# Performance work log

Hardware: AMD Instinct MI355X
Metric: run time of the kernel (lower is better)

Reference implementation:

```python
import jax, jax.numpy as jnp
import numpy as np

B, N, D, H, L = 2, 2048, 512, 8, 2
HD = D // H


def setup_inputs() -> dict:
    key = jax.random.key(0)
    ks = jax.random.split(key, 8)
    s = 0.02
    return {
        "inputs_embeds": jax.random.normal(ks[0], (B, N, D), jnp.float32),
        "pos_emb": jax.random.normal(ks[1], (N, D), jnp.float32) * s,
        "c_attn_w": jax.random.normal(ks[2], (L, D, 3 * D), jnp.float32) * s,
        "c_attn_b": jnp.zeros((L, 3 * D), jnp.float32),
        "out_w": jax.random.normal(ks[3], (L, D, D), jnp.float32) * s,
        "out_b": jnp.zeros((L, D), jnp.float32),
        "ln1_g": jnp.ones((L, D), jnp.float32),
        "ln1_b": jnp.zeros((L, D), jnp.float32),
        "c_fc_w": jax.random.normal(ks[4], (L, D, 4 * D), jnp.float32) * s,
        "c_fc_b": jnp.zeros((L, 4 * D), jnp.float32),
        "c_proj_w": jax.random.normal(ks[5], (L, 4 * D, D), jnp.float32) * s,
        "c_proj_b": jnp.zeros((L, D), jnp.float32),
        "ln2_g": jnp.ones((L, D), jnp.float32),
        "ln2_b": jnp.zeros((L, D), jnp.float32),
    }


def _layernorm(x, g, b, eps=1e-5):
    mu = jnp.mean(x, axis=-1, keepdims=True)
    var = jnp.mean(jnp.square(x - mu), axis=-1, keepdims=True)
    return (x - mu) * jax.lax.rsqrt(var + eps) * g + b


def _gelu_new(x):
    # NewGELUActivation: tanh approximation
    return 0.5 * x * (1.0 + jnp.tanh(jnp.sqrt(2.0 / jnp.pi) * (x + 0.044715 * x ** 3)))


def _attention(x, w_qkv, b_qkv, w_out, b_out, self_mask):
    qkv = x @ w_qkv + b_qkv                      # [B,N,3D]
    q, k, v = jnp.split(qkv, 3, axis=-1)
    def heads(t):
        return t.reshape(B, N, H, HD).transpose(0, 2, 1, 3)  # [B,H,N,HD]
    q, k, v = heads(q), heads(k), heads(v)
    scores = jnp.einsum('bhqd,bhkd->bhqk', q, k) / jnp.sqrt(jnp.float32(HD))
    neg = jnp.finfo(scores.dtype).min
    scores = jnp.where(self_mask, scores, neg)   # exclude-self mask
    attn = jax.nn.softmax(scores, axis=-1)
    o = jnp.einsum('bhqk,bhkd->bhqd', attn, v)
    o = o.transpose(0, 2, 1, 3).reshape(B, N, D)
    return o @ w_out + b_out


def reference(inputs_embeds, pos_emb, c_attn_w, c_attn_b, out_w, out_b,
              ln1_g, ln1_b, c_fc_w, c_fc_b, c_proj_w, c_proj_b, ln2_g, ln2_b):
    self_mask = ~jnp.eye(N, dtype=bool)[None, None]  # [1,1,N,N]
    h = inputs_embeds + pos_emb[None]
    for l in range(L):
        res = h
        x = _layernorm(h, ln1_g[l], ln1_b[l])
        h = _attention(x, c_attn_w[l], c_attn_b[l], out_w[l], out_b[l], self_mask) + res
        res = h
        x = _layernorm(h, ln2_g[l], ln2_b[l])
        x = _gelu_new(x @ c_fc_w[l] + c_fc_b[l])
        h = (x @ c_proj_w[l] + c_proj_b[l]) + res
    return h
```

## Files before the change

kernel.cpp:

```cpp
#include <hip/hip_runtime.h>
#include <hip/hip_bf16.h>
#include <math.h>

#define BB 2
#define NN 2048
#define DD 512
#define HH 8
#define LL 2
#define TT (BB*NN)

typedef short short8 __attribute__((ext_vector_type(8)));
typedef float floatx4 __attribute__((ext_vector_type(4)));

__device__ __forceinline__ unsigned short f2b(float v) {
    union { float f; unsigned u; } x; x.f = v;
    unsigned r = x.u + 0x7fff + ((x.u >> 16) & 1);
    return (unsigned short)(r >> 16);
}

__device__ __forceinline__ unsigned fbits(float v) {
    union { float f; unsigned u; } x; x.f = v; return x.u;
}

__device__ __forceinline__ unsigned pk_bf16_rtz(float a, float b) {
#if __has_builtin(__builtin_amdgcn_perm)
    return __builtin_amdgcn_perm(fbits(b), fbits(a), 0x07060302);
#else
    return (fbits(b) & 0xFFFF0000u) | (fbits(a) >> 16);
#endif
}

__global__ __launch_bounds__(256) void k_embed(const float* __restrict__ emb,
                                               const float* __restrict__ pos,
                                               float* __restrict__ h) {
    int i = blockIdx.x * 256 + threadIdx.x;
    h[i] = emb[i] + pos[i & (NN * DD - 1)];
}

__global__ __launch_bounds__(256) void k_bias_add(const float* __restrict__ src,
                                                  const float* __restrict__ bias,
                                                  float* __restrict__ dst) {
    int i = blockIdx.x * 256 + threadIdx.x;
    dst[i] = src[i] + bias[i & (DD - 1)];
}

__global__ __launch_bounds__(256) void k_ln(const float* __restrict__ hin,
                                            unsigned short* __restrict__ xout,
                                            const float* __restrict__ g,
                                            const float* __restrict__ b) {
    __shared__ float red[4];
    __shared__ float bc1, bc2;
    int t = blockIdx.x;
    int tid = threadIdx.x;
    int lane = tid & 63, wv = tid >> 6;
    const float* row = hin + (size_t)t * DD;
    float v0 = row[tid];
    float v1 = row[tid + 256];

    float s = v0 + v1;
#pragma unroll
    for (int o = 32; o; o >>= 1) s += __shfl_down(s, o, 64);
    if (lane == 0) red[wv] = s;
    __syncthreads();
    if (tid == 0) bc1 = (red[0] + red[1] + red[2] + red[3]) * (1.0f / DD);
    __syncthreads();
    float mu = bc1;
    float d0 = v0 - mu, d1 = v1 - mu;
    s = d0 * d0 + d1 * d1;
#pragma unroll
    for (int o = 32; o; o >>= 1) s += __shfl_down(s, o, 64);
    if (lane == 0) red[wv] = s;
    __syncthreads();
    if (tid == 0) bc2 = (red[0] + red[1] + red[2] + red[3]) * (1.0f / DD);
    __syncthreads();
    float rstd = rsqrtf(bc2 + 1e-5f);
    xout[(size_t)t * DD + tid]       = f2b(d0 * rstd * g[tid] + b[tid]);
    xout[(size_t)t * DD + tid + 256] = f2b(d1 * rstd * g[tid + 256] + b[tid + 256]);
}

__device__ __forceinline__ float gelu_new(float v) {
    const float c = 0.7978845608028654f;
    float u = c * (v + 0.044715f * v * v * v);
    return 0.5f * v * (1.0f + tanhf(u));
}

#define PL 3145728
__global__ __launch_bounds__(256) void k_wt_all(const float* __restrict__ c_attn_w,
                                                const float* __restrict__ out_w,
                                                const float* __restrict__ c_fc_w,
                                                const float* __restrict__ c_proj_w,
                                                unsigned short* __restrict__ wbuf) {
    __shared__ unsigned short t[64][72];
    int bx = blockIdx.x;
    int l = bx / 768;
    int r = bx - l * 768;
    const float* W; unsigned short* WT; int K, N;
    if (r < 192)      { W = c_attn_w + (size_t)l * 512 * 1536; WT = wbuf + (size_t)l * PL;           K = 512;  N = 1536; }
    else if (r < 256) { r -= 192; W = out_w  + (size_t)l * 512 * 512;  WT = wbuf + (size_t)l * PL + 786432;  K = 512;  N = 512; }
    else if (r < 512) { r -= 256; W = c_fc_w + (size_t)l * 512 * 2048; WT = wbuf + (size_t)l * PL + 1048576; K = 512;  N = 2048; }
    else              { r -= 512; W = c_proj_w + (size_t)l * 2048 * 512; WT = wbuf + (size_t)l * PL + 2097152; K = 2048; N = 512; }
    int tiles_n = N >> 6;
    int n0 = (r % tiles_n) * 64, k0 = (r / tiles_n) * 64;

    int tid = threadIdx.x;
    int rr = tid >> 2;
    int c0 = (tid & 3) * 16;
    const float* src = W + (size_t)(k0 + rr) * N + n0 + c0;
#pragma unroll
    for (int u = 0; u < 4; u++) {
        float4 v = *(const float4*)&src[u * 4];
        t[c0 + u * 4 + 0][rr] = f2b(v.x);
        t[c0 + u * 4 + 1][rr] = f2b(v.y);
        t[c0 + u * 4 + 2][rr] = f2b(v.z);
        t[c0 + u * 4 + 3][rr] = f2b(v.w);
    }
    __syncthreads();
    unsigned short* dst = WT + (size_t)(n0 + rr) * K + k0 + c0;
#pragma unroll
    for (int u = 0; u < 4; u++)
        *(uint2*)&dst[u * 4] = *(const uint2*)&t[rr][c0 + u * 4];
}

template <int ACT, int BF16OUT, int ATOMIC>
__global__ __launch_bounds__(256) void k_mgemm(const unsigned short* __restrict__ Ab,
                                               const unsigned short* __restrict__ Bt,
                                               const float* __restrict__ bias,
                                               float* __restrict__ Cp,
                                               unsigned short* __restrict__ Cb,
                                               int Kfull, int Kchunk, int N) {
    __shared__ unsigned short Als[2][8 * 512];
    __shared__ unsigned short Bls[2][8 * 512];

    int tid = threadIdx.x;
    int l = tid & 63, w = tid >> 6;
    int wm = w >> 1, wn = w & 1;
    int m0 = blockIdx.y * 128, n0 = blockIdx.x * 128;
    int kb = blockIdx.z * Kchunk;
    int lr = l & 15;
    int lk = (l >> 4) * 8;

    const unsigned short* Ap0 = Ab + (size_t)(m0 + (w * 2 + 0) * 16 + lr) * Kfull + kb + lk;
    const unsigned short* Ap1 = Ab + (size_t)(m0 + (w * 2 + 1) * 16 + lr) * Kfull + kb + lk;
    const unsigned short* Bp0 = Bt + (size_t)(n0 + (w * 2 + 0) * 16 + lr) * Kfull + kb + lk;
    const unsigned short* Bp1 = Bt + (size_t)(n0 + (w * 2 + 1) * 16 + lr) * Kfull + kb + lk;
    int la0 = (w * 2 + 0) * 512 + l * 8;
    int la1 = (w * 2 + 1) * 512 + l * 8;

    floatx4 acc[4][4];
#pragma unroll
    for (int i = 0; i < 4; i++)
#pragma unroll
        for (int j = 0; j < 4; j++) acc[i][j] = (floatx4){0.f, 0.f, 0.f, 0.f};

    int nit = Kchunk >> 5;

    uint4 ra0 = *(const uint4*)Ap0;
    uint4 ra1 = *(const uint4*)Ap1;
    uint4 rb0 = *(const uint4*)Bp0;
    uint4 rb1 = *(const uint4*)Bp1;
    *(uint4*)&Als[0][la0] = ra0;
    *(uint4*)&Als[0][la1] = ra1;
    *(uint4*)&Bls[0][la0] = rb0;
    *(uint4*)&Bls[0][la1] = rb1;
    if (nit > 1) {
        ra0 = *(const uint4*)(Ap0 + 32);
        ra1 = *(const uint4*)(Ap1 + 32);
        rb0 = *(const uint4*)(Bp0 + 32);
        rb1 = *(const uint4*)(Bp1 + 32);
    }
    __syncthreads();

    for (int it = 0; it < nit; it++) {
        int c = it & 1;
        if (it + 1 < nit) {
            *(uint4*)&Als[c ^ 1][la0] = ra0;
            *(uint4*)&Als[c ^ 1][la1] = ra1;
            *(uint4*)&Bls[c ^ 1][la0] = rb0;
            *(uint4*)&Bls[c ^ 1][la1] = rb1;
        }
        if (it + 2 < nit) {
            int ko = (it + 2) << 5;
            ra0 = *(const uint4*)(Ap0 + ko);
            ra1 = *(const uint4*)(Ap1 + ko);
            rb0 = *(const uint4*)(Bp0 + ko);
            rb1 = *(const uint4*)(Bp1 + ko);
        }
        short8 a[4], b[4];
#pragma unroll
        for (int i = 0; i < 4; i++) {
            a[i] = *(const short8*)&Als[c][(wm * 4 + i) * 512 + l * 8];
            b[i] = *(const short8*)&Bls[c][(wn * 4 + i) * 512 + l * 8];
        }
#pragma unroll
        for (int i = 0; i < 4; i++)
#pragma unroll
            for (int j = 0; j < 4; j++)
                acc[i][j] = __builtin_amdgcn_mfma_f32_16x16x32_bf16(a[i], b[j], acc[i][j], 0, 0, 0);
        __syncthreads();
    }

    int col_in = l & 15, rquad = (l >> 4) * 4;
    bool addb = (!ATOMIC) || (bias != nullptr && blockIdx.z == 0);
#pragma unroll
    for (int i = 0; i < 4; i++) {
        int gm_base = m0 + wm * 64 + i * 16 + rquad;
#pragma unroll
        for (int j = 0; j < 4; j++) {
            int gn = n0 + wn * 64 + j * 16 + col_in;
            float bv = addb ? bias[gn] : 0.0f;
#pragma unroll
            for (int r = 0; r < 4; r++) {
                size_t off = (size_t)(gm_base + r) * N + gn;
                if (ATOMIC) {
                    atomicAdd(&Cp[off], acc[i][j][r] + bv);
                } else {
                    float v = acc[i][j][r] + bv;
                    if (ACT) v = gelu_new(v);
                    if (BF16OUT) Cb[off] = f2b(v);
                    else Cp[off] = v;
                }
            }
        }
    }
}

__global__ __launch_bounds__(256) void k_attn_mfma(const unsigned short* __restrict__ qkv,
                                                   unsigned short* __restrict__ xatt) {
    __shared__ unsigned short Ks[2][64 * 72];
    __shared__ unsigned short Vt[2][64 * 72];
    __shared__ unsigned short Pls[64 * 72];

    int qt = blockIdx.x, hd = blockIdx.y, b = blockIdx.z;
    int tid = threadIdx.x;
    int l = tid & 63, w = tid >> 6;
    int lr = l & 15, quad = l >> 4;

    const size_t base = (size_t)b * NN * 1536;

    short8 qf[2];
    {
        const unsigned short* qrow = qkv + base + (size_t)(qt * 64 + w * 16 + lr) * 1536 + hd * 64;
        qf[0] = *(const short8*)&qrow[quad * 8];
        qf[1] = *(const short8*)&qrow[quad * 8 + 32];
    }
    short8 onef;
#pragma unroll
    for (int i = 0; i < 8; i++) onef[i] = (short)0x3F80;

    floatx4 O[4];
#pragma unroll
    for (int jd = 0; jd < 4; jd++) O[jd] = (floatx4){0.f, 0.f, 0.f, 0.f};
    floatx4 sacc = (floatx4){0.f, 0.f, 0.f, 0.f};

    int sr = tid >> 2, sc = (tid & 3) * 16;
    int vk = (tid & 15) * 4, vd = (tid >> 4) * 4;
    const unsigned short* Kbase = qkv + base + 512 + hd * 64;
    const unsigned short* Vbase = qkv + base + 1024 + hd * 64;

    uint4 rk0 = *(const uint4*)&Kbase[(size_t)sr * 1536 + sc];
    uint4 rk1 = *(const uint4*)&Kbase[(size_t)sr * 1536 + sc + 8];
    union { uint2 u; unsigned short s[4]; } rv[4];
#pragma unroll
    for (int i = 0; i < 4; i++)
        rv[i].u = *(const uint2*)&Vbase[(size_t)(vk + i) * 1536 + vd];
    *(uint4*)&Ks[0][sr * 72 + sc]     = rk0;
    *(uint4*)&Ks[0][sr * 72 + sc + 8] = rk1;
#pragma unroll
    for (int j = 0; j < 4; j++) {
        union { uint2 u; unsigned short s[4]; } pk;
        pk.s[0] = rv[0].s[j]; pk.s[1] = rv[1].s[j];
        pk.s[2] = rv[2].s[j]; pk.s[3] = rv[3].s[j];
        *(uint2*)&Vt[0][(vd + j) * 72 + vk] = pk.u;
    }
    {
        rk0 = *(const uint4*)&Kbase[(size_t)(64 + sr) * 1536 + sc];
        rk1 = *(const uint4*)&Kbase[(size_t)(64 + sr) * 1536 + sc + 8];
#pragma unroll
        for (int i = 0; i < 4; i++)
            rv[i].u = *(const uint2*)&Vbase[(size_t)(64 + vk + i) * 1536 + vd];
    }
    __syncthreads();

    const float C1 = 0.18033688f;
    const float C2 = -11.5415603f;
    int mq = w * 16 + lr;

    for (int kt = 0; kt < 32; kt++) {
        int c = kt & 1;
        if (kt < 31) {
            *(uint4*)&Ks[c ^ 1][sr * 72 + sc]     = rk0;
            *(uint4*)&Ks[c ^ 1][sr * 72 + sc + 8] = rk1;
#pragma unroll
            for (int j = 0; j < 4; j++) {
                union { uint2 u; unsigned short s[4]; } pk;
                pk.s[0] = rv[0].s[j]; pk.s[1] = rv[1].s[j];
                pk.s[2] = rv[2].s[j]; pk.s[3] = rv[3].s[j];
                *(uint2*)&Vt[c ^ 1][(vd + j) * 72 + vk] = pk.u;
            }
        }
        if (kt < 30) {
            int kn = (kt + 2) * 64;
            rk0 = *(const uint4*)&Kbase[(size_t)(kn + sr) * 1536 + sc];
            rk1 = *(const uint4*)&Kbase[(size_t)(kn + sr) * 1536 + sc + 8];
#pragma unroll
            for (int i = 0; i < 4; i++)
                rv[i].u = *(const uint2*)&Vbase[(size_t)(kn + vk + i) * 1536 + vd];
        }

        floatx4 s[4];
#pragma unroll
        for (int jn = 0; jn < 4; jn++) s[jn] = (floatx4){0.f, 0.f, 0.f, 0.f};
#pragma unroll
        for (int ss = 0; ss < 2; ss++)
#pragma unroll
            for (int jn = 0; jn < 4; jn++) {
                short8 ak = *(const short8*)&Ks[c][(jn * 16 + lr) * 72 + ss * 32 + quad * 8];
                s[jn] = __builtin_amdgcn_mfma_f32_16x16x32_bf16(ak, qf[ss], s[jn], 0, 0, 0);
            }

#pragma unroll
        for (int jn = 0; jn < 4; jn++) {
            float p[4];
#pragma unroll
            for (int r = 0; r < 4; r++) {
                p[r] = exp2f(fmaf(s[jn][r], C1, C2));
                if (kt == qt && mq == jn * 16 + quad * 4 + r) p[r] = 0.0f;
            }
            uint2 pk;
            pk.x = pk_bf16_rtz(p[0], p[1]);
            pk.y = pk_bf16_rtz(p[2], p[3]);
            *(uint2*)&Pls[mq * 72 + jn * 16 + quad * 4] = pk;
        }

#pragma unroll
        for (int ss = 0; ss < 2; ss++) {
            short8 ap = *(const short8*)&Pls[(w * 16 + lr) * 72 + ss * 32 + quad * 8];
#pragma unroll
            for (int jd = 0; jd < 4; jd++) {
                short8 bv = *(const short8*)&Vt[c][(jd * 16 + lr) * 72 + ss * 32 + quad * 8];
                O[jd] = __builtin_amdgcn_mfma_f32_16x16x32_bf16(ap, bv, O[jd], 0, 0, 0);
            }
            sacc = __builtin_amdgcn_mfma_f32_16x16x32_bf16(ap, onef, sacc, 0, 0, 0);
        }
        __syncthreads();
    }

#pragma unroll
    for (int r = 0; r < 4; r++) {
        float inv = 1.0f / sacc[r];
        size_t tok = (size_t)b * NN + qt * 64 + w * 16 + quad * 4 + r;
#pragma unroll
        for (int jd = 0; jd < 4; jd++)
            xatt[tok * DD + hd * 64 + jd * 16 + lr] = f2b(O[jd][r] * inv);
    }
}

extern "C" void kernel_launch(void* const* d_in, const int* in_sizes, int n_in,
                              void* d_out, int out_size, void* d_ws, size_t ws_size,
                              hipStream_t stream) {
    const float* emb      = (const float*)d_in[0];
    const float* pos      = (const float*)d_in[1];
    const float* c_attn_w = (const float*)d_in[2];
    const float* c_attn_b = (const float*)d_in[3];
    const float* out_w    = (const float*)d_in[4];
    const float* out_b    = (const float*)d_in[5];
    const float* ln1_g    = (const float*)d_in[6];
    const float* ln1_b    = (const float*)d_in[7];
    const float* c_fc_w   = (const float*)d_in[8];
    const float* c_fc_b   = (const float*)d_in[9];
    const float* c_proj_w = (const float*)d_in[10];
    const float* c_proj_b = (const float*)d_in[11];
    const float* ln2_g    = (const float*)d_in[12];
    const float* ln2_b    = (const float*)d_in[13];

    char* p = (char*)d_ws;
    float* h = (float*)p;                       p += (size_t)TT * DD * 4;
    unsigned short* act = (unsigned short*)p;   p += (size_t)TT * 2048 * 2;
    unsigned short* x = (unsigned short*)p;     p += (size_t)TT * DD * 2;
    unsigned short* xatt = (unsigned short*)p;  p += (size_t)TT * DD * 2;
    unsigned short* wbuf = (unsigned short*)p;

    unsigned short* qkvb = act;
    unsigned short* ffa  = act;
    float* out = (float*)d_out;

    k_embed<<<TT * DD / 256, 256, 0, stream>>>(emb, pos, h);
    k_wt_all<<<1536, 256, 0, stream>>>(c_attn_w, out_w, c_fc_w, c_proj_w, wbuf);

    for (int l = 0; l < LL; l++) {
        unsigned short* wqkv_t  = wbuf + (size_t)l * PL;
        unsigned short* wout_t  = wqkv_t + 786432;
        unsigned short* wfc_t   = wqkv_t + 1048576;
        unsigned short* wproj_t = wqkv_t + 2097152;

        k_ln<<<TT, 256, 0, stream>>>(h, x, ln1_g + l * DD, ln1_b + l * DD);
        k_mgemm<0, 1, 0><<<dim3(1536 / 128, TT / 128), 256, 0, stream>>>(
            x, wqkv_t, c_attn_b + l * 1536, nullptr, qkvb, 512, 512, 1536);
        k_attn_mfma<<<dim3(NN / 64, HH, BB), 256, 0, stream>>>(qkvb, xatt);
        k_mgemm<0, 0, 1><<<dim3(512 / 128, TT / 128, 2), 256, 0, stream>>>(
            xatt, wout_t, out_b + l * DD, h, nullptr, 512, 256, 512);
        k_ln<<<TT, 256, 0, stream>>>(h, x, ln2_g + l * DD, ln2_b + l * DD);
        k_mgemm<1, 1, 0><<<dim3(2048 / 128, TT / 128), 256, 0, stream>>>(
            x, wfc_t, c_fc_b + l * 2048, nullptr, ffa, 512, 512, 2048);
        if (l == LL - 1) {
            k_bias_add<<<TT * DD / 256, 256, 0, stream>>>(h, c_proj_b + l * DD, out);
            k_mgemm<0, 0, 1><<<dim3(512 / 128, TT / 128, 4), 256, 0, stream>>>(
                ffa, wproj_t, nullptr, out, nullptr, 2048, 512, 512);
        } else {
            k_mgemm<0, 0, 1><<<dim3(512 / 128, TT / 128, 4), 256, 0, stream>>>(
                ffa, wproj_t, c_proj_b + l * DD, h, nullptr, 2048, 512, 512);
        }
    }
}
```

Measured before the change: 442.5 us.

## Fuse embed into first LN, split-K QKV with bf16 atomics, single-buffer attention

Folds the embedding plus positional add into the first layernorm kernel, which also writes h, so one launch and one pass over h disappear. The QKV GEMM becomes split-K over two z-slices that accumulate into a zeroed bf16 buffer with packed bf16 atomic adds, adding a memset and extra atomic traffic with bf16 rounding in the partial sums. The attention kernel drops the double-buffered K/V shared tiles for a single buffer with two barriers per iteration, lowering LDS use but exposing load latency.

```diff
diff --git a/kernel.cpp b/kernel.cpp
--- a/kernel.cpp
+++ b/kernel.cpp
@@ -18,6 +18,10 @@
     return (unsigned short)(r >> 16);
 }
 
+__device__ __forceinline__ float b2f(unsigned short b) {
+    union { unsigned u; float f; } x; x.u = ((unsigned)b) << 16; return x.f;
+}
+
 __device__ __forceinline__ unsigned fbits(float v) {
     union { float f; unsigned u; } x; x.f = v; return x.u;
 }
@@ -30,11 +34,24 @@
 #endif
 }
 
-__global__ __launch_bounds__(256) void k_embed(const float* __restrict__ emb,
-                                               const float* __restrict__ pos,
-                                               float* __restrict__ h) {
-    int i = blockIdx.x * 256 + threadIdx.x;
-    h[i] = emb[i] + pos[i & (NN * DD - 1)];
+__device__ __forceinline__ void atomic_pk_add_bf16(unsigned short* p, float lo, float hi) {
+#if __has_builtin(__builtin_amdgcn_global_atomic_fadd_v2bf16)
+    typedef short s2 __attribute__((ext_vector_type(2)));
+    s2 v;
+    v[0] = (short)f2b(lo);
+    v[1] = (short)f2b(hi);
+    __builtin_amdgcn_global_atomic_fadd_v2bf16((__attribute__((address_space(1))) s2*)p, v);
+#else
+    unsigned* a = (unsigned*)p;
+    unsigned old = *a, assumed;
+    do {
+        assumed = old;
+        float nlo = b2f((unsigned short)(assumed & 0xffff)) + lo;
+        float nhi = b2f((unsigned short)(assumed >> 16)) + hi;
+        unsigned nv = ((unsigned)f2b(nhi) << 16) | (unsigned)f2b(nlo);
+        old = atomicCAS(a, assumed, nv);
+    } while (old != assumed);
+#endif
 }
 
 __global__ __launch_bounds__(256) void k_bias_add(const float* __restrict__ src,
@@ -44,18 +61,32 @@
     dst[i] = src[i] + bias[i & (DD - 1)];
 }
 
+template <int EMB>
 __global__ __launch_bounds__(256) void k_ln(const float* __restrict__ hin,
                                             unsigned short* __restrict__ xout,
                                             const float* __restrict__ g,
-                                            const float* __restrict__ b) {
+                                            const float* __restrict__ b,
+                                            const float* __restrict__ emb,
+                                            const float* __restrict__ pos,
+                                            float* __restrict__ hout) {
     __shared__ float red[4];
     __shared__ float bc1, bc2;
     int t = blockIdx.x;
     int tid = threadIdx.x;
     int lane = tid & 63, wv = tid >> 6;
-    const float* row = hin + (size_t)t * DD;
-    float v0 = row[tid];
-    float v1 = row[tid + 256];
+    float v0, v1;
+    if (EMB) {
+        const float* erow = emb + (size_t)t * DD;
+        const float* prow = pos + (size_t)(t & (NN - 1)) * DD;
+        v0 = erow[tid] + prow[tid];
+        v1 = erow[tid + 256] + prow[tid + 256];
+        hout[(size_t)t * DD + tid] = v0;
+        hout[(size_t)t * DD + tid + 256] = v1;
+    } else {
+        const float* row = hin + (size_t)t * DD;
+        v0 = row[tid];
+        v1 = row[tid + 256];
+    }
 
     float s = v0 + v1;
 #pragma unroll
@@ -200,7 +231,7 @@
     }
 
     int col_in = l & 15, rquad = (l >> 4) * 4;
-    bool addb = (!ATOMIC) || (bias != nullptr && blockIdx.z == 0);
+    bool addb = (ATOMIC == 0) || (bias != nullptr && blockIdx.z == 0);
 #pragma unroll
     for (int i = 0; i < 4; i++) {
         int gm_base = m0 + wm * 64 + i * 16 + rquad;
@@ -211,8 +242,13 @@
 #pragma unroll
             for (int r = 0; r < 4; r++) {
                 size_t off = (size_t)(gm_base + r) * N + gn;
-                if (ATOMIC) {
+                if (ATOMIC == 1) {
                     atomicAdd(&Cp[off], acc[i][j][r] + bv);
+                } else if (ATOMIC == 2) {
+                    float v = acc[i][j][r] + bv;
+                    float pv = __shfl_xor(v, 1);
+                    if ((l & 1) == 0)
+                        atomic_pk_add_bf16(&Cb[off], v, pv);
                 } else {
                     float v = acc[i][j][r] + bv;
                     if (ACT) v = gelu_new(v);
@@ -226,8 +262,8 @@
 
 __global__ __launch_bounds__(256) void k_attn_mfma(const unsigned short* __restrict__ qkv,
                                                    unsigned short* __restrict__ xatt) {
-    __shared__ unsigned short Ks[2][64 * 72];
-    __shared__ unsigned short Vt[2][64 * 72];
+    __shared__ unsigned short Ks[64 * 72];
+    __shared__ unsigned short Vt[64 * 72];
     __shared__ unsigned short Pls[64 * 72];
 
     int qt = blockIdx.x, hd = blockIdx.y, b = blockIdx.z;
@@ -257,49 +293,32 @@
     const unsigned short* Kbase = qkv + base + 512 + hd * 64;
     const unsigned short* Vbase = qkv + base + 1024 + hd * 64;
 
-    uint4 rk0 = *(const uint4*)&Kbase[(size_t)sr * 1536 + sc];
-    uint4 rk1 = *(const uint4*)&Kbase[(size_t)sr * 1536 + sc + 8];
+    uint4 rk0, rk1;
     union { uint2 u; unsigned short s[4]; } rv[4];
+    rk0 = *(const uint4*)&Kbase[(size_t)sr * 1536 + sc];
+    rk1 = *(const uint4*)&Kbase[(size_t)sr * 1536 + sc + 8];
 #pragma unroll
     for (int i = 0; i < 4; i++)
         rv[i].u = *(const uint2*)&Vbase[(size_t)(vk + i) * 1536 + vd];
-    *(uint4*)&Ks[0][sr * 72 + sc]     = rk0;
-    *(uint4*)&Ks[0][sr * 72 + sc + 8] = rk1;
-#pragma unroll
-    for (int j = 0; j < 4; j++) {
-        union { uint2 u; unsigned short s[4]; } pk;
-        pk.s[0] = rv[0].s[j]; pk.s[1] = rv[1].s[j];
-        pk.s[2] = rv[2].s[j]; pk.s[3] = rv[3].s[j];
-        *(uint2*)&Vt[0][(vd + j) * 72 + vk] = pk.u;
-    }
-    {
-        rk0 = *(const uint4*)&Kbase[(size_t)(64 + sr) * 1536 + sc];
-        rk1 = *(const uint4*)&Kbase[(size_t)(64 + sr) * 1536 + sc + 8];
-#pragma unroll
-        for (int i = 0; i < 4; i++)
-            rv[i].u = *(const uint2*)&Vbase[(size_t)(64 + vk + i) * 1536 + vd];
-    }
-    __syncthreads();
 
     const float C1 = 0.18033688f;
     const float C2 = -11.5415603f;
     int mq = w * 16 + lr;
 
     for (int kt = 0; kt < 32; kt++) {
-        int c = kt & 1;
+        __syncthreads();
+        *(uint4*)&Ks[sr * 72 + sc]     = rk0;
+        *(uint4*)&Ks[sr * 72 + sc + 8] = rk1;
+#pragma unroll
+        for (int j = 0; j < 4; j++) {
+            union { uint2 u; unsigned short s[4]; } pk;
+            pk.s[0] = rv[0].s[j]; pk.s[1] = rv[1].s[j];
+            pk.s[2] = rv[2].s[j]; pk.s[3] = rv[3].s[j];
+            *(uint2*)&Vt[(vd + j) * 72 + vk] = pk.u;
+        }
+        __syncthreads();
         if (kt < 31) {
-            *(uint4*)&Ks[c ^ 1][sr * 72 + sc]     = rk0;
-            *(uint4*)&Ks[c ^ 1][sr * 72 + sc + 8] = rk1;
-#pragma unroll
-            for (int j = 0; j < 4; j++) {
-                union { uint2 u; unsigned short s[4]; } pk;
-                pk.s[0] = rv[0].s[j]; pk.s[1] = rv[1].s[j];
-                pk.s[2] = rv[2].s[j]; pk.s[3] = rv[3].s[j];
-                *(uint2*)&Vt[c ^ 1][(vd + j) * 72 + vk] = pk.u;
-            }
-        }
-        if (kt < 30) {
-            int kn = (kt + 2) * 64;
+            int kn = (kt + 1) * 64;
             rk0 = *(const uint4*)&Kbase[(size_t)(kn + sr) * 1536 + sc];
             rk1 = *(const uint4*)&Kbase[(size_t)(kn + sr) * 1536 + sc + 8];
 #pragma unroll
@@ -314,7 +333,7 @@
         for (int ss = 0; ss < 2; ss++)
 #pragma unroll
             for (int jn = 0; jn < 4; jn++) {
-                short8 ak = *(const short8*)&Ks[c][(jn * 16 + lr) * 72 + ss * 32 + quad * 8];
+                short8 ak = *(const short8*)&Ks[(jn * 16 + lr) * 72 + ss * 32 + quad * 8];
                 s[jn] = __builtin_amdgcn_mfma_f32_16x16x32_bf16(ak, qf[ss], s[jn], 0, 0, 0);
             }
 
@@ -337,12 +356,11 @@
             short8 ap = *(const short8*)&Pls[(w * 16 + lr) * 72 + ss * 32 + quad * 8];
 #pragma unroll
             for (int jd = 0; jd < 4; jd++) {
-                short8 bv = *(const short8*)&Vt[c][(jd * 16 + lr) * 72 + ss * 32 + quad * 8];
+                short8 bv = *(const short8*)&Vt[(jd * 16 + lr) * 72 + ss * 32 + quad * 8];
                 O[jd] = __builtin_amdgcn_mfma_f32_16x16x32_bf16(ap, bv, O[jd], 0, 0, 0);
             }
             sacc = __builtin_amdgcn_mfma_f32_16x16x32_bf16(ap, onef, sacc, 0, 0, 0);
         }
-        __syncthreads();
     }
 
 #pragma unroll
@@ -384,7 +402,6 @@
     unsigned short* ffa  = act;
     float* out = (float*)d_out;
 
-    k_embed<<<TT * DD / 256, 256, 0, stream>>>(emb, pos, h);
     k_wt_all<<<1536, 256, 0, stream>>>(c_attn_w, out_w, c_fc_w, c_proj_w, wbuf);
 
     for (int l = 0; l < LL; l++) {
@@ -393,13 +410,19 @@
         unsigned short* wfc_t   = wqkv_t + 1048576;
         unsigned short* wproj_t = wqkv_t + 2097152;
 
-        k_ln<<<TT, 256, 0, stream>>>(h, x, ln1_g + l * DD, ln1_b + l * DD);
-        k_mgemm<0, 1, 0><<<dim3(1536 / 128, TT / 128), 256, 0, stream>>>(
-            x, wqkv_t, c_attn_b + l * 1536, nullptr, qkvb, 512, 512, 1536);
+        if (l == 0)
+            k_ln<1><<<TT, 256, 0, stream>>>(nullptr, x, ln1_g, ln1_b, emb, pos, h);
+        else
+            k_ln<0><<<TT, 256, 0, stream>>>(h, x, ln1_g + l * DD, ln1_b + l * DD,
+                                            nullptr, nullptr, nullptr);
+        hipMemsetAsync(qkvb, 0, (size_t)TT * 1536 * 2, stream);
+        k_mgemm<0, 0, 2><<<dim3(1536 / 128, TT / 128, 2), 256, 0, stream>>>(
+            x, wqkv_t, c_attn_b + l * 1536, nullptr, qkvb, 512, 256, 1536);
         k_attn_mfma<<<dim3(NN / 64, HH, BB), 256, 0, stream>>>(qkvb, xatt);
         k_mgemm<0, 0, 1><<<dim3(512 / 128, TT / 128, 2), 256, 0, stream>>>(
             xatt, wout_t, out_b + l * DD, h, nullptr, 512, 256, 512);
-        k_ln<<<TT, 256, 0, stream>>>(h, x, ln2_g + l * DD, ln2_b + l * DD);
+        k_ln<0><<<TT, 256, 0, stream>>>(h, x, ln2_g + l * DD, ln2_b + l * DD,
+                                        nullptr, nullptr, nullptr);
         k_mgemm<1, 1, 0><<<dim3(2048 / 128, TT / 128), 256, 0, stream>>>(
             x, wfc_t, c_fc_b + l * 2048, nullptr, ffa, 512, 512, 2048);
         if (l == LL - 1) {
```

After: 523.2 us. 18.2% more time.
